# Performance work log

Hardware: AMD Instinct MI355X
Metric: run time of the kernel (lower is better)

The kernel has to match this reference:

```python
import jax, jax.numpy as jnp
import numpy as np

B, L, C, N = 64, 512, 1, 128  # batch, max seq len, num_conjugates, num_tags


def setup_inputs() -> dict:
    key = jax.random.key(0)
    k1, k2, k3, k4, k5 = jax.random.split(key, 5)
    emissions = jax.random.normal(k1, (B, L, C, N), dtype=jnp.float32)
    transitions = jax.random.normal(k2, (C, N, N), dtype=jnp.float32) * 0.01
    start_transitions = jax.random.normal(k3, (C, N), dtype=jnp.float32) * 0.01
    end_transitions = jax.random.normal(k4, (C, N), dtype=jnp.float32) * 0.01
    lengths = jax.random.randint(k5, (B,), 1, L + 1)  # valid lengths in [1, L]
    return {
        "emissions": emissions,
        "transitions": transitions,
        "start_transitions": start_transitions,
        "end_transitions": end_transitions,
        "lengths": lengths,
    }


def reference(emissions, transitions, start_transitions, end_transitions, lengths):
    # CRF log-partition (forward algorithm in the log semiring).
    # emissions: [B, L, C, N]; transitions: [C, N, N]; start/end: [C, N]; lengths: [B]
    b, l, c, n = emissions.shape
    # alpha_0 = start + emission at t=0  -> [B, C, N]
    alpha0 = start_transitions[None, :, :] + emissions[:, 0]

    e_rest = jnp.moveaxis(emissions[:, 1:], 1, 0)  # [L-1, B, C, N]
    t_idx = jnp.arange(1, l)

    def step(alpha, inp):
        e_t, t = inp
        # log-semiring mat-vec: logsumexp over previous tag axis
        scores = alpha[..., :, None] + transitions[None] + e_t[..., None, :]  # [B,C,N,N]
        new_alpha = jax.nn.logsumexp(scores, axis=2)  # [B, C, N]
        active = (t < lengths)[:, None, None]  # ragged mask: freeze finished sequences
        return jnp.where(active, new_alpha, alpha), None

    alpha, _ = jax.lax.scan(step, alpha0, (e_rest, t_idx))
    # terminate with end transitions -> log partition per (batch, conjugate)
    return jax.nn.logsumexp(alpha + end_transitions[None, :, :], axis=-1)  # [B, C]
```

## Files before the change

kernel.cpp:

```cpp
#include <hip/hip_runtime.h>


#define LOG2E 1.4426950408889634f
#define LN2   0.6931471805599453f

#define LDS_BARRIER() asm volatile("s_waitcnt lgkmcnt(0)\n\ts_barrier" ::: "memory")

typedef float    f2 __attribute__((ext_vector_type(2)));
typedef _Float16 h2 __attribute__((ext_vector_type(2)));

#define PKRTZ(a, b) __builtin_bit_cast(h2, __builtin_amdgcn_cvt_pkrtz((a), (b)))

template <int CTRL>
__device__ __forceinline__ float dpp_f(float x) {
    return __int_as_float(
        __builtin_amdgcn_mov_dpp(__float_as_int(x), CTRL, 0xF, 0xF, false));
}

__global__ __launch_bounds__(256)
__attribute__((amdgpu_waves_per_eu(1, 1)))
void crf_halves(
    const float* __restrict__ emissions,
    const float* __restrict__ transitions,
    const float* __restrict__ start_t,
    const float* __restrict__ end_t,
    const int*   __restrict__ lengths,
    float* __restrict__ wsV,
    int*   __restrict__ wsO)
{
    constexpr int N = 128;
    constexpr int L = 512;
    const int  bid = blockIdx.x;
    const bool isf = bid < 64;
    const int  b   = isf ? bid : bid - 64;
    const int  tid = threadIdx.x;
    const int  g   = tid >> 2;
    const int  k   = tid & 3;

    __shared__ alignas(16) float pbuf[2][80];

    h2 EA_0,  EA_1,  EA_2,  EA_3,  EA_4,  EA_5,  EA_6,  EA_7;
    h2 EA_8,  EA_9,  EA_10, EA_11, EA_12, EA_13, EA_14, EA_15;
    h2 EB_0,  EB_1,  EB_2,  EB_3,  EB_4,  EB_5,  EB_6,  EB_7;
    h2 EB_8,  EB_9,  EB_10, EB_11, EB_12, EB_13, EB_14, EB_15;
    if (isf) {
        const float* tb = transitions + (size_t)(32 * k) * N + 2 * g;
#define INIT_F(m)                                                              \
        {                                                                      \
            f2 r0 = *reinterpret_cast<const f2*>(tb + (size_t)(2 * (m)) * N);  \
            f2 r1 = *reinterpret_cast<const f2*>(tb + (size_t)(2 * (m) + 1) * N); \
            EA_##m = PKRTZ(__builtin_amdgcn_exp2f(r0.x * LOG2E),               \
                           __builtin_amdgcn_exp2f(r1.x * LOG2E));              \
            EB_##m = PKRTZ(__builtin_amdgcn_exp2f(r0.y * LOG2E),               \
                           __builtin_amdgcn_exp2f(r1.y * LOG2E));              \
        }
        INIT_F(0)  INIT_F(1)  INIT_F(2)  INIT_F(3)
        INIT_F(4)  INIT_F(5)  INIT_F(6)  INIT_F(7)
        INIT_F(8)  INIT_F(9)  INIT_F(10) INIT_F(11)
        INIT_F(12) INIT_F(13) INIT_F(14) INIT_F(15)
#undef INIT_F
    } else {
        const float* ra_ = transitions + (size_t)(2 * g) * N + 32 * k;
        const float* rb_ = transitions + (size_t)(2 * g + 1) * N + 32 * k;
#define INIT_B(m)                                                              \
        {                                                                      \
            f2 r0 = *reinterpret_cast<const f2*>(ra_ + 2 * (m));               \
            f2 r1 = *reinterpret_cast<const f2*>(rb_ + 2 * (m));               \
            EA_##m = PKRTZ(__builtin_amdgcn_exp2f(r0.x * LOG2E),               \
                           __builtin_amdgcn_exp2f(r0.y * LOG2E));              \
            EB_##m = PKRTZ(__builtin_amdgcn_exp2f(r1.x * LOG2E),               \
                           __builtin_amdgcn_exp2f(r1.y * LOG2E));              \
        }
        INIT_B(0)  INIT_B(1)  INIT_B(2)  INIT_B(3)
        INIT_B(4)  INIT_B(5)  INIT_B(6)  INIT_B(7)
        INIT_B(8)  INIT_B(9)  INIT_B(10) INIT_B(11)
        INIT_B(12) INIT_B(13) INIT_B(14) INIT_B(15)
#undef INIT_B
    }

    const int len = lengths[b];
    const int m   = (len - 1) >> 1;
    const float* eb = emissions + (size_t)b * L * N;

    int n_steps, e0, dstep; bool zfinal;
    if (isf) {
        n_steps = m; e0 = 1; dstep = 1; zfinal = false;
    } else {
        int total = len - 1 - m;
        n_steps = total > 0 ? total - 1 : 0;
        e0 = len - 2; if (e0 < 0) e0 = 0;
        dstep = -1;
        zfinal = total > 0;
    }

    int o = 0, cur = 0;
    float qA, qB;
    {
        const float* base = isf ? start_t : end_t;
        f2 bt = *reinterpret_cast<const f2*>(base + 2 * g);
        f2 ev;
        if (isf)         ev = *reinterpret_cast<const f2*>(eb + 2 * g);
        else if (zfinal) ev = *reinterpret_cast<const f2*>(eb + (size_t)(len - 1) * N + 2 * g);
        else           { ev.x = 0.f; ev.y = 0.f; }
        qA = __builtin_amdgcn_exp2f((bt.x + ev.x) * LOG2E);
        qB = __builtin_amdgcn_exp2f((bt.y + ev.y) * LOG2E);
        if (k == 0)
            pbuf[0][(g >> 4) * 20 + (g & 15)] =
                __builtin_bit_cast(float, PKRTZ(qA, qB));
    }
    LDS_BARRIER();

    auto eidx = [&](int n) {
        int nn = (n < n_steps) ? n : (n_steps - 1);
        if (nn < 0) nn = 0;
        return e0 + dstep * nn;
    };
    auto ldE = [&](int tt) {
        return *reinterpret_cast<const f2*>(eb + (size_t)tt * N + 2 * g);
    };

    auto STEP = [&](f2 ecur) {
        float q0w = pbuf[cur][0];
        const float4* pv = reinterpret_cast<const float4*>(&pbuf[cur][k * 20]);
        float4 Q0 = pv[0], Q1 = pv[1], Q2 = pv[2], Q3 = pv[3];

        unsigned u0 = __float_as_uint(q0w);
        int eS = (int)((u0 >> 10) & 0x1Fu) - 15;
        o += eS;
        float feS = (float)eS;
        float esA = __builtin_amdgcn_exp2f(ecur.x * LOG2E - feS);
        float esB = __builtin_amdgcn_exp2f(ecur.y * LOG2E - feS);

        float aA0 = 0.f, aA1 = 0.f, aB0 = 0.f, aB1 = 0.f;
#define D0(m_, Qc)                                                             \
        {                                                                      \
            h2 pm = __builtin_bit_cast(h2, Qc);                                \
            aA0 = __builtin_amdgcn_fdot2(pm, EA_##m_, aA0, false);             \
            aB0 = __builtin_amdgcn_fdot2(pm, EB_##m_, aB0, false);             \
        }
#define D1(m_, Qc)                                                             \
        {                                                                      \
            h2 pm = __builtin_bit_cast(h2, Qc);                                \
            aA1 = __builtin_amdgcn_fdot2(pm, EA_##m_, aA1, false);             \
            aB1 = __builtin_amdgcn_fdot2(pm, EB_##m_, aB1, false);             \
        }
        D0(0,  Q0.x) D1(1,  Q0.y) D0(2,  Q0.z) D1(3,  Q0.w)
        D0(4,  Q1.x) D1(5,  Q1.y) D0(6,  Q1.z) D1(7,  Q1.w)
        D0(8,  Q2.x) D1(9,  Q2.y) D0(10, Q2.z) D1(11, Q2.w)
        D0(12, Q3.x) D1(13, Q3.y) D0(14, Q3.z) D1(15, Q3.w)
#undef D0
#undef D1
        float dA = aA0 + aA1;
        float dB = aB0 + aB1;

        dA += dpp_f<0xB1>(dA); dB += dpp_f<0xB1>(dB);
        dA += dpp_f<0x4E>(dA); dB += dpp_f<0x4E>(dB);

        qA = esA * dA;
        qB = esB * dB;
        cur ^= 1;
        if (k == 0)
            pbuf[cur][(g >> 4) * 20 + (g & 15)] =
                __builtin_bit_cast(float, PKRTZ(qA, qB));
        LDS_BARRIER();
    };

    f2 ra = ldE(eidx(0));
    f2 rb = ldE(eidx(1));
    f2 rc = ldE(eidx(2));
    f2 rd = ldE(eidx(3));

    int n = 0;
    while (n < n_steps) {
        STEP(ra); ra = ldE(eidx(n + 4)); ++n; if (n >= n_steps) break;
        STEP(rb); rb = ldE(eidx(n + 4)); ++n; if (n >= n_steps) break;
        STEP(rc); rc = ldE(eidx(n + 4)); ++n; if (n >= n_steps) break;
        STEP(rd); rd = ldE(eidx(n + 4)); ++n;
    }
    if (zfinal) {
        f2 z; z.x = 0.f; z.y = 0.f;
        STEP(z);
    }

    float* wv = wsV + (size_t)((isf ? 0 : 64) + b) * 128;
    if (k == 0) {
        f2 q; q.x = qA; q.y = qB;
        *reinterpret_cast<f2*>(wv + 2 * g) = q;
    }
    if (tid == 0) wsO[(isf ? 0 : 64) + b] = o;
}

__global__ __launch_bounds__(64)
void crf_combine(const float* __restrict__ wsV, const int* __restrict__ wsO,
                 const int* __restrict__ lengths, float* __restrict__ out)
{
    const int b = blockIdx.x;
    const int g = threadIdx.x;
    f2 a = *reinterpret_cast<const f2*>(wsV + (size_t)b * 128 + 2 * g);
    f2 x = *reinterpret_cast<const f2*>(wsV + (size_t)(64 + b) * 128 + 2 * g);
    float v = a.x * x.x + a.y * x.y;
    #pragma unroll
    for (int s = 1; s < 64; s <<= 1) v += __shfl_xor(v, s);
    if (g == 0)
        out[b] = LN2 * ((float)(wsO[b] + wsO[64 + b]) +
                        __builtin_amdgcn_logf(v));
}

extern "C" void kernel_launch(void* const* d_in, const int* in_sizes, int n_in,
                              void* d_out, int out_size, void* d_ws, size_t ws_size,
                              hipStream_t stream) {
    const float* emissions   = (const float*)d_in[0];
    const float* transitions = (const float*)d_in[1];
    const float* start_t     = (const float*)d_in[2];
    const float* end_t       = (const float*)d_in[3];
    const int*   lengths     = (const int*)d_in[4];
    float* out = (float*)d_out;

    float* wsV = (float*)d_ws;
    int*   wsO = (int*)((char*)d_ws + 2 * 64 * 128 * sizeof(float));

    crf_halves<<<dim3(128), dim3(256), 0, stream>>>(
        emissions, transitions, start_t, end_t, lengths, wsV, wsO);
    crf_combine<<<dim3(64), dim3(64), 0, stream>>>(wsV, wsO, lengths, out);
}
```

Measured before the change: 131.5 us.

## Run each CRF half-chain in a single wavefront without block barriers

Each block shrinks from 256 threads to a single 64-lane wavefront. Every lane now holds all 64 fp16 transition pairs for its two tags and performs the full 128-term dot product itself, which replaces the DPP cross-lane reduction and the s_barrier with a plain LDS waitcnt, since a single wave needs no block barrier. The aim is to shorten the serial per-step latency chain. In exchange each lane does 4x more fdot2 work and reads all 64 packed alphas from LDS every step. The 128 transition registers per lane also raise register pressure and the risk of spilling.

```diff
diff --git a/kernel.cpp b/kernel.cpp
--- a/kernel.cpp
+++ b/kernel.cpp
@@ -4,20 +4,15 @@
 #define LOG2E 1.4426950408889634f
 #define LN2   0.6931471805599453f
 
-#define LDS_BARRIER() asm volatile("s_waitcnt lgkmcnt(0)\n\ts_barrier" ::: "memory")
+#define LGKM0() asm volatile("s_waitcnt lgkmcnt(0)" ::: "memory")
 
 typedef float    f2 __attribute__((ext_vector_type(2)));
+typedef float    f4 __attribute__((ext_vector_type(4)));
 typedef _Float16 h2 __attribute__((ext_vector_type(2)));
 
 #define PKRTZ(a, b) __builtin_bit_cast(h2, __builtin_amdgcn_cvt_pkrtz((a), (b)))
 
-template <int CTRL>
-__device__ __forceinline__ float dpp_f(float x) {
-    return __int_as_float(
-        __builtin_amdgcn_mov_dpp(__float_as_int(x), CTRL, 0xF, 0xF, false));
-}
-
-__global__ __launch_bounds__(256)
+__global__ __launch_bounds__(64)
 __attribute__((amdgpu_waves_per_eu(1, 1)))
 void crf_halves(
     const float* __restrict__ emissions,
@@ -33,49 +28,34 @@
     const int  bid = blockIdx.x;
     const bool isf = bid < 64;
     const int  b   = isf ? bid : bid - 64;
-    const int  tid = threadIdx.x;
-    const int  g   = tid >> 2;
-    const int  k   = tid & 3;
+    const int  p   = threadIdx.x;
 
-    __shared__ alignas(16) float pbuf[2][80];
+    __shared__ alignas(16) float pbuf[2][64];
 
-    h2 EA_0,  EA_1,  EA_2,  EA_3,  EA_4,  EA_5,  EA_6,  EA_7;
-    h2 EA_8,  EA_9,  EA_10, EA_11, EA_12, EA_13, EA_14, EA_15;
-    h2 EB_0,  EB_1,  EB_2,  EB_3,  EB_4,  EB_5,  EB_6,  EB_7;
-    h2 EB_8,  EB_9,  EB_10, EB_11, EB_12, EB_13, EB_14, EB_15;
+    h2 EA[64], EB[64];
     if (isf) {
-        const float* tb = transitions + (size_t)(32 * k) * N + 2 * g;
-#define INIT_F(m)                                                              \
-        {                                                                      \
-            f2 r0 = *reinterpret_cast<const f2*>(tb + (size_t)(2 * (m)) * N);  \
-            f2 r1 = *reinterpret_cast<const f2*>(tb + (size_t)(2 * (m) + 1) * N); \
-            EA_##m = PKRTZ(__builtin_amdgcn_exp2f(r0.x * LOG2E),               \
-                           __builtin_amdgcn_exp2f(r1.x * LOG2E));              \
-            EB_##m = PKRTZ(__builtin_amdgcn_exp2f(r0.y * LOG2E),               \
-                           __builtin_amdgcn_exp2f(r1.y * LOG2E));              \
+        const float* tb = transitions + 2 * p;
+        #pragma unroll
+        for (int m = 0; m < 64; ++m) {
+            f2 r0 = *reinterpret_cast<const f2*>(tb + (size_t)(2 * m) * N);
+            f2 r1 = *reinterpret_cast<const f2*>(tb + (size_t)(2 * m + 1) * N);
+            EA[m] = PKRTZ(__builtin_amdgcn_exp2f(r0.x * LOG2E),
+                          __builtin_amdgcn_exp2f(r1.x * LOG2E));
+            EB[m] = PKRTZ(__builtin_amdgcn_exp2f(r0.y * LOG2E),
+                          __builtin_amdgcn_exp2f(r1.y * LOG2E));
         }
-        INIT_F(0)  INIT_F(1)  INIT_F(2)  INIT_F(3)
-        INIT_F(4)  INIT_F(5)  INIT_F(6)  INIT_F(7)
-        INIT_F(8)  INIT_F(9)  INIT_F(10) INIT_F(11)
-        INIT_F(12) INIT_F(13) INIT_F(14) INIT_F(15)
-#undef INIT_F
     } else {
-        const float* ra_ = transitions + (size_t)(2 * g) * N + 32 * k;
-        const float* rb_ = transitions + (size_t)(2 * g + 1) * N + 32 * k;
-#define INIT_B(m)                                                              \
-        {                                                                      \
-            f2 r0 = *reinterpret_cast<const f2*>(ra_ + 2 * (m));               \
-            f2 r1 = *reinterpret_cast<const f2*>(rb_ + 2 * (m));               \
-            EA_##m = PKRTZ(__builtin_amdgcn_exp2f(r0.x * LOG2E),               \
-                           __builtin_amdgcn_exp2f(r0.y * LOG2E));              \
-            EB_##m = PKRTZ(__builtin_amdgcn_exp2f(r1.x * LOG2E),               \
-                           __builtin_amdgcn_exp2f(r1.y * LOG2E));              \
+        const float* ra_ = transitions + (size_t)(2 * p) * N;
+        const float* rb_ = ra_ + N;
+        #pragma unroll
+        for (int m = 0; m < 64; ++m) {
+            f2 r0 = *reinterpret_cast<const f2*>(ra_ + 2 * m);
+            f2 r1 = *reinterpret_cast<const f2*>(rb_ + 2 * m);
+            EA[m] = PKRTZ(__builtin_amdgcn_exp2f(r0.x * LOG2E),
+                          __builtin_amdgcn_exp2f(r0.y * LOG2E));
+            EB[m] = PKRTZ(__builtin_amdgcn_exp2f(r1.x * LOG2E),
+                          __builtin_amdgcn_exp2f(r1.y * LOG2E));
         }
-        INIT_B(0)  INIT_B(1)  INIT_B(2)  INIT_B(3)
-        INIT_B(4)  INIT_B(5)  INIT_B(6)  INIT_B(7)
-        INIT_B(8)  INIT_B(9)  INIT_B(10) INIT_B(11)
-        INIT_B(12) INIT_B(13) INIT_B(14) INIT_B(15)
-#undef INIT_B
     }
 
     const int len = lengths[b];
@@ -97,18 +77,16 @@
     float qA, qB;
     {
         const float* base = isf ? start_t : end_t;
-        f2 bt = *reinterpret_cast<const f2*>(base + 2 * g);
+        f2 bt = *reinterpret_cast<const f2*>(base + 2 * p);
         f2 ev;
-        if (isf)         ev = *reinterpret_cast<const f2*>(eb + 2 * g);
-        else if (zfinal) ev = *reinterpret_cast<const f2*>(eb + (size_t)(len - 1) * N + 2 * g);
+        if (isf)         ev = *reinterpret_cast<const f2*>(eb + 2 * p);
+        else if (zfinal) ev = *reinterpret_cast<const f2*>(eb + (size_t)(len - 1) * N + 2 * p);
         else           { ev.x = 0.f; ev.y = 0.f; }
         qA = __builtin_amdgcn_exp2f((bt.x + ev.x) * LOG2E);
         qB = __builtin_amdgcn_exp2f((bt.y + ev.y) * LOG2E);
-        if (k == 0)
-            pbuf[0][(g >> 4) * 20 + (g & 15)] =
-                __builtin_bit_cast(float, PKRTZ(qA, qB));
+        pbuf[0][p] = __builtin_bit_cast(float, PKRTZ(qA, qB));
     }
-    LDS_BARRIER();
+    LGKM0();
 
     auto eidx = [&](int n) {
         int nn = (n < n_steps) ? n : (n_steps - 1);
@@ -116,53 +94,38 @@
         return e0 + dstep * nn;
     };
     auto ldE = [&](int tt) {
-        return *reinterpret_cast<const f2*>(eb + (size_t)tt * N + 2 * g);
+        return *reinterpret_cast<const f2*>(eb + (size_t)tt * N + 2 * p);
     };
 
     auto STEP = [&](f2 ecur) {
-        float q0w = pbuf[cur][0];
-        const float4* pv = reinterpret_cast<const float4*>(&pbuf[cur][k * 20]);
-        float4 Q0 = pv[0], Q1 = pv[1], Q2 = pv[2], Q3 = pv[3];
+        const f4* pv = reinterpret_cast<const f4*>(&pbuf[cur][0]);
+        f4 P[16];
+        #pragma unroll
+        for (int r = 0; r < 16; ++r) P[r] = pv[r];
 
-        unsigned u0 = __float_as_uint(q0w);
+        unsigned u0 = __float_as_uint(P[0][0]);
         int eS = (int)((u0 >> 10) & 0x1Fu) - 15;
         o += eS;
         float feS = (float)eS;
         float esA = __builtin_amdgcn_exp2f(ecur.x * LOG2E - feS);
         float esB = __builtin_amdgcn_exp2f(ecur.y * LOG2E - feS);
 
-        float aA0 = 0.f, aA1 = 0.f, aB0 = 0.f, aB1 = 0.f;
-#define D0(m_, Qc)                                                             \
-        {                                                                      \
-            h2 pm = __builtin_bit_cast(h2, Qc);                                \
-            aA0 = __builtin_amdgcn_fdot2(pm, EA_##m_, aA0, false);             \
-            aB0 = __builtin_amdgcn_fdot2(pm, EB_##m_, aB0, false);             \
+        float aA[4] = {0.f, 0.f, 0.f, 0.f};
+        float aB[4] = {0.f, 0.f, 0.f, 0.f};
+        #pragma unroll
+        for (int mm = 0; mm < 64; ++mm) {
+            h2 pm = __builtin_bit_cast(h2, P[mm >> 2][mm & 3]);
+            aA[mm & 3] = __builtin_amdgcn_fdot2(pm, EA[mm], aA[mm & 3], false);
+            aB[mm & 3] = __builtin_amdgcn_fdot2(pm, EB[mm], aB[mm & 3], false);
         }
-#define D1(m_, Qc)                                                             \
-        {                                                                      \
-            h2 pm = __builtin_bit_cast(h2, Qc);                                \
-            aA1 = __builtin_amdgcn_fdot2(pm, EA_##m_, aA1, false);             \
-            aB1 = __builtin_amdgcn_fdot2(pm, EB_##m_, aB1, false);             \
-        }
-        D0(0,  Q0.x) D1(1,  Q0.y) D0(2,  Q0.z) D1(3,  Q0.w)
-        D0(4,  Q1.x) D1(5,  Q1.y) D0(6,  Q1.z) D1(7,  Q1.w)
-        D0(8,  Q2.x) D1(9,  Q2.y) D0(10, Q2.z) D1(11, Q2.w)
-        D0(12, Q3.x) D1(13, Q3.y) D0(14, Q3.z) D1(15, Q3.w)
-#undef D0
-#undef D1
-        float dA = aA0 + aA1;
-        float dB = aB0 + aB1;
-
-        dA += dpp_f<0xB1>(dA); dB += dpp_f<0xB1>(dB);
-        dA += dpp_f<0x4E>(dA); dB += dpp_f<0x4E>(dB);
+        float dA = (aA[0] + aA[1]) + (aA[2] + aA[3]);
+        float dB = (aB[0] + aB[1]) + (aB[2] + aB[3]);
 
         qA = esA * dA;
         qB = esB * dB;
         cur ^= 1;
-        if (k == 0)
-            pbuf[cur][(g >> 4) * 20 + (g & 15)] =
-                __builtin_bit_cast(float, PKRTZ(qA, qB));
-        LDS_BARRIER();
+        pbuf[cur][p] = __builtin_bit_cast(float, PKRTZ(qA, qB));
+        LGKM0();
     };
 
     f2 ra = ldE(eidx(0));
@@ -183,11 +146,9 @@
     }
 
     float* wv = wsV + (size_t)((isf ? 0 : 64) + b) * 128;
-    if (k == 0) {
-        f2 q; q.x = qA; q.y = qB;
-        *reinterpret_cast<f2*>(wv + 2 * g) = q;
-    }
-    if (tid == 0) wsO[(isf ? 0 : 64) + b] = o;
+    f2 q; q.x = qA; q.y = qB;
+    *reinterpret_cast<f2*>(wv + 2 * p) = q;
+    if (p == 0) wsO[(isf ? 0 : 64) + b] = o;
 }
 
 __global__ __launch_bounds__(64)
@@ -219,7 +180,7 @@
     float* wsV = (float*)d_ws;
     int*   wsO = (int*)((char*)d_ws + 2 * 64 * 128 * sizeof(float));
 
-    crf_halves<<<dim3(128), dim3(256), 0, stream>>>(
+    crf_halves<<<dim3(128), dim3(64), 0, stream>>>(
         emissions, transitions, start_t, end_t, lengths, wsV, wsO);
     crf_combine<<<dim3(64), dim3(64), 0, stream>>>(wsV, wsO, lengths, out);
 }
```

New measurement: 228.3 us. 73.6% more time.

## Interleave two batch sequences per block to hide per-step barrier latency

Applied to the files above, without the earlier changes.

Each block now advances two independent batch sequences (b and b+32) in lockstep. They share one LDS barrier per step and their dot-product chains are interleaved, so the latency-bound recurrence gets twice the independent work between barriers. The grid drops from 128 to 64 blocks. The loop now runs to the longer of the two sequences, so the shorter one idles under per-round guards, and the extra live registers add pressure.

```diff
diff --git a/kernel.cpp b/kernel.cpp
--- a/kernel.cpp
+++ b/kernel.cpp
@@ -31,13 +31,16 @@
     constexpr int N = 128;
     constexpr int L = 512;
     const int  bid = blockIdx.x;
-    const bool isf = bid < 64;
-    const int  b   = isf ? bid : bid - 64;
+    const bool isf = bid < 32;
+    const int  s   = isf ? bid : bid - 32;
+    const int  b1  = s;
+    const int  b2  = s + 32;
     const int  tid = threadIdx.x;
     const int  g   = tid >> 2;
     const int  k   = tid & 3;
 
-    __shared__ alignas(16) float pbuf[2][80];
+    __shared__ alignas(16) float pb1[2][80];
+    __shared__ alignas(16) float pb2[2][80];
 
     h2 EA_0,  EA_1,  EA_2,  EA_3,  EA_4,  EA_5,  EA_6,  EA_7;
     h2 EA_8,  EA_9,  EA_10, EA_11, EA_12, EA_13, EA_14, EA_15;
@@ -78,116 +81,163 @@
 #undef INIT_B
     }
 
-    const int len = lengths[b];
-    const int m   = (len - 1) >> 1;
-    const float* eb = emissions + (size_t)b * L * N;
-
-    int n_steps, e0, dstep; bool zfinal;
+    const int len1 = lengths[b1];
+    const int len2 = lengths[b2];
+    const int m1   = (len1 - 1) >> 1;
+    const int m2   = (len2 - 1) >> 1;
+    const float* eb1 = emissions + (size_t)b1 * L * N;
+    const float* eb2 = emissions + (size_t)b2 * L * N;
+
+    int ns1, e01, total1, ns2, e02, total2, dstep;
     if (isf) {
-        n_steps = m; e0 = 1; dstep = 1; zfinal = false;
+        dstep = 1;
+        ns1 = m1; e01 = 1; total1 = m1;
+        ns2 = m2; e02 = 1; total2 = m2;
     } else {
-        int total = len - 1 - m;
-        n_steps = total > 0 ? total - 1 : 0;
-        e0 = len - 2; if (e0 < 0) e0 = 0;
         dstep = -1;
-        zfinal = total > 0;
-    }
-
-    int o = 0, cur = 0;
-    float qA, qB;
+        int tt1 = len1 - 1 - m1;
+        ns1 = tt1 > 0 ? tt1 - 1 : 0; e01 = len1 - 2 < 0 ? 0 : len1 - 2; total1 = tt1;
+        int tt2 = len2 - 1 - m2;
+        ns2 = tt2 > 0 ? tt2 - 1 : 0; e02 = len2 - 2 < 0 ? 0 : len2 - 2; total2 = tt2;
+    }
+
+    int o1 = 0, o2 = 0, cur = 0;
+    float qA1, qB1, qA2, qB2;
     {
         const float* base = isf ? start_t : end_t;
         f2 bt = *reinterpret_cast<const f2*>(base + 2 * g);
-        f2 ev;
-        if (isf)         ev = *reinterpret_cast<const f2*>(eb + 2 * g);
-        else if (zfinal) ev = *reinterpret_cast<const f2*>(eb + (size_t)(len - 1) * N + 2 * g);
-        else           { ev.x = 0.f; ev.y = 0.f; }
-        qA = __builtin_amdgcn_exp2f((bt.x + ev.x) * LOG2E);
-        qB = __builtin_amdgcn_exp2f((bt.y + ev.y) * LOG2E);
-        if (k == 0)
-            pbuf[0][(g >> 4) * 20 + (g & 15)] =
-                __builtin_bit_cast(float, PKRTZ(qA, qB));
+        f2 ev1, ev2;
+        if (isf) {
+            ev1 = *reinterpret_cast<const f2*>(eb1 + 2 * g);
+            ev2 = *reinterpret_cast<const f2*>(eb2 + 2 * g);
+        } else {
+            if (len1 > 1) ev1 = *reinterpret_cast<const f2*>(eb1 + (size_t)(len1 - 1) * N + 2 * g);
+            else        { ev1.x = 0.f; ev1.y = 0.f; }
+            if (len2 > 1) ev2 = *reinterpret_cast<const f2*>(eb2 + (size_t)(len2 - 1) * N + 2 * g);
+            else        { ev2.x = 0.f; ev2.y = 0.f; }
+        }
+        qA1 = __builtin_amdgcn_exp2f((bt.x + ev1.x) * LOG2E);
+        qB1 = __builtin_amdgcn_exp2f((bt.y + ev1.y) * LOG2E);
+        qA2 = __builtin_amdgcn_exp2f((bt.x + ev2.x) * LOG2E);
+        qB2 = __builtin_amdgcn_exp2f((bt.y + ev2.y) * LOG2E);
+        if (k == 0) {
+            pb1[0][(g >> 4) * 20 + (g & 15)] = __builtin_bit_cast(float, PKRTZ(qA1, qB1));
+            pb2[0][(g >> 4) * 20 + (g & 15)] = __builtin_bit_cast(float, PKRTZ(qA2, qB2));
+        }
     }
     LDS_BARRIER();
 
-    auto eidx = [&](int n) {
-        int nn = (n < n_steps) ? n : (n_steps - 1);
+    auto ei1 = [&](int n) {
+        int nn = (n < ns1) ? n : (ns1 - 1);
         if (nn < 0) nn = 0;
-        return e0 + dstep * nn;
-    };
-    auto ldE = [&](int tt) {
-        return *reinterpret_cast<const f2*>(eb + (size_t)tt * N + 2 * g);
-    };
-
-    auto STEP = [&](f2 ecur) {
-        float q0w = pbuf[cur][0];
-        const float4* pv = reinterpret_cast<const float4*>(&pbuf[cur][k * 20]);
-        float4 Q0 = pv[0], Q1 = pv[1], Q2 = pv[2], Q3 = pv[3];
-
-        unsigned u0 = __float_as_uint(q0w);
-        int eS = (int)((u0 >> 10) & 0x1Fu) - 15;
-        o += eS;
-        float feS = (float)eS;
-        float esA = __builtin_amdgcn_exp2f(ecur.x * LOG2E - feS);
-        float esB = __builtin_amdgcn_exp2f(ecur.y * LOG2E - feS);
-
+        return e01 + dstep * nn;
+    };
+    auto ei2 = [&](int n) {
+        int nn = (n < ns2) ? n : (ns2 - 1);
+        if (nn < 0) nn = 0;
+        return e02 + dstep * nn;
+    };
+    auto ldE1 = [&](int tt) {
+        return *reinterpret_cast<const f2*>(eb1 + (size_t)tt * N + 2 * g);
+    };
+    auto ldE2 = [&](int tt) {
+        return *reinterpret_cast<const f2*>(eb2 + (size_t)tt * N + 2 * g);
+    };
+
+    auto DOT = [&](const float4& Qa, const float4& Qb, const float4& Qc,
+                   const float4& Qd, float& dA, float& dB) {
         float aA0 = 0.f, aA1 = 0.f, aB0 = 0.f, aB1 = 0.f;
-#define D0(m_, Qc)                                                             \
-        {                                                                      \
-            h2 pm = __builtin_bit_cast(h2, Qc);                                \
+#define D0(m_, Qc_)                                                            \
+        {                                                                      \
+            h2 pm = __builtin_bit_cast(h2, Qc_);                               \
             aA0 = __builtin_amdgcn_fdot2(pm, EA_##m_, aA0, false);             \
             aB0 = __builtin_amdgcn_fdot2(pm, EB_##m_, aB0, false);             \
         }
-#define D1(m_, Qc)                                                             \
-        {                                                                      \
-            h2 pm = __builtin_bit_cast(h2, Qc);                                \
+#define D1(m_, Qc_)                                                            \
+        {                                                                      \
+            h2 pm = __builtin_bit_cast(h2, Qc_);                               \
             aA1 = __builtin_amdgcn_fdot2(pm, EA_##m_, aA1, false);             \
             aB1 = __builtin_amdgcn_fdot2(pm, EB_##m_, aB1, false);             \
         }
-        D0(0,  Q0.x) D1(1,  Q0.y) D0(2,  Q0.z) D1(3,  Q0.w)
-        D0(4,  Q1.x) D1(5,  Q1.y) D0(6,  Q1.z) D1(7,  Q1.w)
-        D0(8,  Q2.x) D1(9,  Q2.y) D0(10, Q2.z) D1(11, Q2.w)
-        D0(12, Q3.x) D1(13, Q3.y) D0(14, Q3.z) D1(15, Q3.w)
+        D0(0,  Qa.x) D1(1,  Qa.y) D0(2,  Qa.z) D1(3,  Qa.w)
+        D0(4,  Qb.x) D1(5,  Qb.y) D0(6,  Qb.z) D1(7,  Qb.w)
+        D0(8,  Qc.x) D1(9,  Qc.y) D0(10, Qc.z) D1(11, Qc.w)
+        D0(12, Qd.x) D1(13, Qd.y) D0(14, Qd.z) D1(15, Qd.w)
 #undef D0
 #undef D1
-        float dA = aA0 + aA1;
-        float dB = aB0 + aB1;
-
-        dA += dpp_f<0xB1>(dA); dB += dpp_f<0xB1>(dB);
-        dA += dpp_f<0x4E>(dA); dB += dpp_f<0x4E>(dB);
-
-        qA = esA * dA;
-        qB = esB * dB;
+        float dA_ = aA0 + aA1;
+        float dB_ = aB0 + aB1;
+        dA_ += dpp_f<0xB1>(dA_); dB_ += dpp_f<0xB1>(dB_);
+        dA_ += dpp_f<0x4E>(dA_); dB_ += dpp_f<0x4E>(dB_);
+        dA = dA_; dB = dB_;
+    };
+
+    auto ROUND = [&](f2 e1, f2 e2, int r) {
+        float q0w1 = pb1[cur][0];
+        const float4* pv1 = reinterpret_cast<const float4*>(&pb1[cur][k * 20]);
+        float4 Qa1 = pv1[0], Qb1 = pv1[1], Qc1 = pv1[2], Qd1 = pv1[3];
+        float q0w2 = pb2[cur][0];
+        const float4* pv2 = reinterpret_cast<const float4*>(&pb2[cur][k * 20]);
+        float4 Qa2 = pv2[0], Qb2 = pv2[1], Qc2 = pv2[2], Qd2 = pv2[3];
+
+        float dA1, dB1, dA2, dB2;
+        DOT(Qa1, Qb1, Qc1, Qd1, dA1, dB1);
+        DOT(Qa2, Qb2, Qc2, Qd2, dA2, dB2);
+
+        if (r < total1) {
+            unsigned u0 = __float_as_uint(q0w1);
+            int eS = (int)((u0 >> 10) & 0x1Fu) - 15;
+            o1 += eS;
+            float feS = (float)eS;
+            f2 ec = e1;
+            if (r >= ns1) { ec.x = 0.f; ec.y = 0.f; }
+            qA1 = __builtin_amdgcn_exp2f(ec.x * LOG2E - feS) * dA1;
+            qB1 = __builtin_amdgcn_exp2f(ec.y * LOG2E - feS) * dB1;
+        }
+        if (r < total2) {
+            unsigned u0 = __float_as_uint(q0w2);
+            int eS = (int)((u0 >> 10) & 0x1Fu) - 15;
+            o2 += eS;
+            float feS = (float)eS;
+            f2 ec = e2;
+            if (r >= ns2) { ec.x = 0.f; ec.y = 0.f; }
+            qA2 = __builtin_amdgcn_exp2f(ec.x * LOG2E - feS) * dA2;
+            qB2 = __builtin_amdgcn_exp2f(ec.y * LOG2E - feS) * dB2;
+        }
         cur ^= 1;
-        if (k == 0)
-            pbuf[cur][(g >> 4) * 20 + (g & 15)] =
-                __builtin_bit_cast(float, PKRTZ(qA, qB));
+        if (k == 0) {
+            pb1[cur][(g >> 4) * 20 + (g & 15)] = __builtin_bit_cast(float, PKRTZ(qA1, qB1));
+            pb2[cur][(g >> 4) * 20 + (g & 15)] = __builtin_bit_cast(float, PKRTZ(qA2, qB2));
+        }
         LDS_BARRIER();
     };
 
-    f2 ra = ldE(eidx(0));
-    f2 rb = ldE(eidx(1));
-    f2 rc = ldE(eidx(2));
-    f2 rd = ldE(eidx(3));
-
-    int n = 0;
-    while (n < n_steps) {
-        STEP(ra); ra = ldE(eidx(n + 4)); ++n; if (n >= n_steps) break;
-        STEP(rb); rb = ldE(eidx(n + 4)); ++n; if (n >= n_steps) break;
-        STEP(rc); rc = ldE(eidx(n + 4)); ++n; if (n >= n_steps) break;
-        STEP(rd); rd = ldE(eidx(n + 4)); ++n;
-    }
-    if (zfinal) {
-        f2 z; z.x = 0.f; z.y = 0.f;
-        STEP(z);
-    }
-
-    float* wv = wsV + (size_t)((isf ? 0 : 64) + b) * 128;
-    if (k == 0) {
-        f2 q; q.x = qA; q.y = qB;
-        *reinterpret_cast<f2*>(wv + 2 * g) = q;
-    }
-    if (tid == 0) wsO[(isf ? 0 : 64) + b] = o;
+    f2 ra1 = ldE1(ei1(0)), rb1 = ldE1(ei1(1)), rc1 = ldE1(ei1(2)), rd1 = ldE1(ei1(3));
+    f2 ra2 = ldE2(ei2(0)), rb2 = ldE2(ei2(1)), rc2 = ldE2(ei2(2)), rd2 = ldE2(ei2(3));
+
+    const int R = total1 > total2 ? total1 : total2;
+    int r = 0;
+    while (r < R) {
+        ROUND(ra1, ra2, r); ra1 = ldE1(ei1(r + 4)); ra2 = ldE2(ei2(r + 4)); ++r; if (r >= R) break;
+        ROUND(rb1, rb2, r); rb1 = ldE1(ei1(r + 4)); rb2 = ldE2(ei2(r + 4)); ++r; if (r >= R) break;
+        ROUND(rc1, rc2, r); rc1 = ldE1(ei1(r + 4)); rc2 = ldE2(ei2(r + 4)); ++r; if (r >= R) break;
+        ROUND(rd1, rd2, r); rd1 = ldE1(ei1(r + 4)); rd2 = ldE2(ei2(r + 4)); ++r;
+    }
+
+    {
+        float* wv1 = wsV + (size_t)((isf ? 0 : 64) + b1) * 128;
+        float* wv2 = wsV + (size_t)((isf ? 0 : 64) + b2) * 128;
+        if (k == 0) {
+            f2 q1; q1.x = qA1; q1.y = qB1;
+            f2 q2; q2.x = qA2; q2.y = qB2;
+            *reinterpret_cast<f2*>(wv1 + 2 * g) = q1;
+            *reinterpret_cast<f2*>(wv2 + 2 * g) = q2;
+        }
+        if (tid == 0) {
+            wsO[(isf ? 0 : 64) + b1] = o1;
+            wsO[(isf ? 0 : 64) + b2] = o2;
+        }
+    }
 }
 
 __global__ __launch_bounds__(64)
@@ -219,7 +269,7 @@
     float* wsV = (float*)d_ws;
     int*   wsO = (int*)((char*)d_ws + 2 * 64 * 128 * sizeof(float));
 
-    crf_halves<<<dim3(128), dim3(256), 0, stream>>>(
+    crf_halves<<<dim3(64), dim3(256), 0, stream>>>(
         emissions, transitions, start_t, end_t, lengths, wsV, wsO);
     crf_combine<<<dim3(64), dim3(64), 0, stream>>>(wsV, wsO, lengths, out);
 }
```

After: 184.1 us. 40.1% more time.

## Remap CRF step so each wave owns a k-slice and reduces partials via LDS

Applied to the files above, without the earlier changes.

Work is remapped so each of the four waves owns a 32-row slice of the previous-tag axis and each lane owns two output tags. The previous alpha vector is gathered with ds_bpermute from the lane's own packed fp16 value instead of being broadcast through LDS. Cross-wave partial sums are then combined through one LDS write, a barrier and vector reads, replacing the DPP quad reduction. The goal is to shorten the per-step serial critical path (LDS store, barrier, LDS load), at the cost of 16 bpermutes per step and a larger LDS reduction buffer.

```diff
diff --git a/kernel.cpp b/kernel.cpp
--- a/kernel.cpp
+++ b/kernel.cpp
@@ -7,15 +7,10 @@
 #define LDS_BARRIER() asm volatile("s_waitcnt lgkmcnt(0)\n\ts_barrier" ::: "memory")
 
 typedef float    f2 __attribute__((ext_vector_type(2)));
+typedef float    f4 __attribute__((ext_vector_type(4)));
 typedef _Float16 h2 __attribute__((ext_vector_type(2)));
 
 #define PKRTZ(a, b) __builtin_bit_cast(h2, __builtin_amdgcn_cvt_pkrtz((a), (b)))
-
-template <int CTRL>
-__device__ __forceinline__ float dpp_f(float x) {
-    return __int_as_float(
-        __builtin_amdgcn_mov_dpp(__float_as_int(x), CTRL, 0xF, 0xF, false));
-}
 
 __global__ __launch_bounds__(256)
 __attribute__((amdgpu_waves_per_eu(1, 1)))
@@ -34,24 +29,24 @@
     const bool isf = bid < 64;
     const int  b   = isf ? bid : bid - 64;
     const int  tid = threadIdx.x;
-    const int  g   = tid >> 2;
-    const int  k   = tid & 3;
-
-    __shared__ alignas(16) float pbuf[2][80];
+    const int  w   = tid >> 6;
+    const int  l   = tid & 63;
+
+    __shared__ alignas(16) float P_red[2][64][8];
 
     h2 EA_0,  EA_1,  EA_2,  EA_3,  EA_4,  EA_5,  EA_6,  EA_7;
     h2 EA_8,  EA_9,  EA_10, EA_11, EA_12, EA_13, EA_14, EA_15;
     h2 EB_0,  EB_1,  EB_2,  EB_3,  EB_4,  EB_5,  EB_6,  EB_7;
     h2 EB_8,  EB_9,  EB_10, EB_11, EB_12, EB_13, EB_14, EB_15;
     if (isf) {
-        const float* tb = transitions + (size_t)(32 * k) * N + 2 * g;
-#define INIT_F(m)                                                              \
+        const float* tb = transitions + (size_t)(32 * w) * N + 2 * l;
+#define INIT_F(j)                                                              \
         {                                                                      \
-            f2 r0 = *reinterpret_cast<const f2*>(tb + (size_t)(2 * (m)) * N);  \
-            f2 r1 = *reinterpret_cast<const f2*>(tb + (size_t)(2 * (m) + 1) * N); \
-            EA_##m = PKRTZ(__builtin_amdgcn_exp2f(r0.x * LOG2E),               \
+            f2 r0 = *reinterpret_cast<const f2*>(tb + (size_t)(2 * (j)) * N);  \
+            f2 r1 = *reinterpret_cast<const f2*>(tb + (size_t)(2 * (j) + 1) * N); \
+            EA_##j = PKRTZ(__builtin_amdgcn_exp2f(r0.x * LOG2E),               \
                            __builtin_amdgcn_exp2f(r1.x * LOG2E));              \
-            EB_##m = PKRTZ(__builtin_amdgcn_exp2f(r0.y * LOG2E),               \
+            EB_##j = PKRTZ(__builtin_amdgcn_exp2f(r0.y * LOG2E),               \
                            __builtin_amdgcn_exp2f(r1.y * LOG2E));              \
         }
         INIT_F(0)  INIT_F(1)  INIT_F(2)  INIT_F(3)
@@ -60,15 +55,15 @@
         INIT_F(12) INIT_F(13) INIT_F(14) INIT_F(15)
 #undef INIT_F
     } else {
-        const float* ra_ = transitions + (size_t)(2 * g) * N + 32 * k;
-        const float* rb_ = transitions + (size_t)(2 * g + 1) * N + 32 * k;
-#define INIT_B(m)                                                              \
+        const float* ra_ = transitions + (size_t)(2 * l) * N + 32 * w;
+        const float* rb_ = transitions + (size_t)(2 * l + 1) * N + 32 * w;
+#define INIT_B(j)                                                              \
         {                                                                      \
-            f2 r0 = *reinterpret_cast<const f2*>(ra_ + 2 * (m));               \
-            f2 r1 = *reinterpret_cast<const f2*>(rb_ + 2 * (m));               \
-            EA_##m = PKRTZ(__builtin_amdgcn_exp2f(r0.x * LOG2E),               \
+            f2 r0 = *reinterpret_cast<const f2*>(ra_ + 2 * (j));               \
+            f2 r1 = *reinterpret_cast<const f2*>(rb_ + 2 * (j));               \
+            EA_##j = PKRTZ(__builtin_amdgcn_exp2f(r0.x * LOG2E),               \
                            __builtin_amdgcn_exp2f(r0.y * LOG2E));              \
-            EB_##m = PKRTZ(__builtin_amdgcn_exp2f(r1.x * LOG2E),               \
+            EB_##j = PKRTZ(__builtin_amdgcn_exp2f(r1.x * LOG2E),               \
                            __builtin_amdgcn_exp2f(r1.y * LOG2E));              \
         }
         INIT_B(0)  INIT_B(1)  INIT_B(2)  INIT_B(3)
@@ -95,20 +90,19 @@
 
     int o = 0, cur = 0;
     float qA, qB;
+    int qpk, sq0;
     {
         const float* base = isf ? start_t : end_t;
-        f2 bt = *reinterpret_cast<const f2*>(base + 2 * g);
+        f2 bt = *reinterpret_cast<const f2*>(base + 2 * l);
         f2 ev;
-        if (isf)         ev = *reinterpret_cast<const f2*>(eb + 2 * g);
-        else if (zfinal) ev = *reinterpret_cast<const f2*>(eb + (size_t)(len - 1) * N + 2 * g);
+        if (isf)         ev = *reinterpret_cast<const f2*>(eb + 2 * l);
+        else if (zfinal) ev = *reinterpret_cast<const f2*>(eb + (size_t)(len - 1) * N + 2 * l);
         else           { ev.x = 0.f; ev.y = 0.f; }
         qA = __builtin_amdgcn_exp2f((bt.x + ev.x) * LOG2E);
         qB = __builtin_amdgcn_exp2f((bt.y + ev.y) * LOG2E);
-        if (k == 0)
-            pbuf[0][(g >> 4) * 20 + (g & 15)] =
-                __builtin_bit_cast(float, PKRTZ(qA, qB));
-    }
-    LDS_BARRIER();
+        qpk = __builtin_bit_cast(int, PKRTZ(qA, qB));
+        sq0 = __builtin_amdgcn_readfirstlane(qpk);
+    }
 
     auto eidx = [&](int n) {
         int nn = (n < n_steps) ? n : (n_steps - 1);
@@ -116,53 +110,62 @@
         return e0 + dstep * nn;
     };
     auto ldE = [&](int tt) {
-        return *reinterpret_cast<const f2*>(eb + (size_t)tt * N + 2 * g);
+        return *reinterpret_cast<const f2*>(eb + (size_t)tt * N + 2 * l);
     };
 
     auto STEP = [&](f2 ecur) {
-        float q0w = pbuf[cur][0];
-        const float4* pv = reinterpret_cast<const float4*>(&pbuf[cur][k * 20]);
-        float4 Q0 = pv[0], Q1 = pv[1], Q2 = pv[2], Q3 = pv[3];
-
-        unsigned u0 = __float_as_uint(q0w);
-        int eS = (int)((u0 >> 10) & 0x1Fu) - 15;
+        int P0  = __builtin_amdgcn_ds_bpermute((16 * w + 0)  * 4, qpk);
+        int P1  = __builtin_amdgcn_ds_bpermute((16 * w + 1)  * 4, qpk);
+        int P2  = __builtin_amdgcn_ds_bpermute((16 * w + 2)  * 4, qpk);
+        int P3  = __builtin_amdgcn_ds_bpermute((16 * w + 3)  * 4, qpk);
+        int P4  = __builtin_amdgcn_ds_bpermute((16 * w + 4)  * 4, qpk);
+        int P5  = __builtin_amdgcn_ds_bpermute((16 * w + 5)  * 4, qpk);
+        int P6  = __builtin_amdgcn_ds_bpermute((16 * w + 6)  * 4, qpk);
+        int P7  = __builtin_amdgcn_ds_bpermute((16 * w + 7)  * 4, qpk);
+        int P8  = __builtin_amdgcn_ds_bpermute((16 * w + 8)  * 4, qpk);
+        int P9  = __builtin_amdgcn_ds_bpermute((16 * w + 9)  * 4, qpk);
+        int P10 = __builtin_amdgcn_ds_bpermute((16 * w + 10) * 4, qpk);
+        int P11 = __builtin_amdgcn_ds_bpermute((16 * w + 11) * 4, qpk);
+        int P12 = __builtin_amdgcn_ds_bpermute((16 * w + 12) * 4, qpk);
+        int P13 = __builtin_amdgcn_ds_bpermute((16 * w + 13) * 4, qpk);
+        int P14 = __builtin_amdgcn_ds_bpermute((16 * w + 14) * 4, qpk);
+        int P15 = __builtin_amdgcn_ds_bpermute((16 * w + 15) * 4, qpk);
+
+        int eS = ((sq0 >> 10) & 31) - 15;
         o += eS;
         float feS = (float)eS;
         float esA = __builtin_amdgcn_exp2f(ecur.x * LOG2E - feS);
         float esB = __builtin_amdgcn_exp2f(ecur.y * LOG2E - feS);
 
         float aA0 = 0.f, aA1 = 0.f, aB0 = 0.f, aB1 = 0.f;
-#define D0(m_, Qc)                                                             \
+#define DJ(j0, j1, Pa, Pb)                                                     \
         {                                                                      \
-            h2 pm = __builtin_bit_cast(h2, Qc);                                \
-            aA0 = __builtin_amdgcn_fdot2(pm, EA_##m_, aA0, false);             \
-            aB0 = __builtin_amdgcn_fdot2(pm, EB_##m_, aB0, false);             \
+            h2 pa = __builtin_bit_cast(h2, Pa);                                \
+            h2 pb = __builtin_bit_cast(h2, Pb);                                \
+            aA0 = __builtin_amdgcn_fdot2(pa, EA_##j0, aA0, false);             \
+            aB0 = __builtin_amdgcn_fdot2(pa, EB_##j0, aB0, false);             \
+            aA1 = __builtin_amdgcn_fdot2(pb, EA_##j1, aA1, false);             \
+            aB1 = __builtin_amdgcn_fdot2(pb, EB_##j1, aB1, false);             \
         }
-#define D1(m_, Qc)                                                             \
-        {                                                                      \
-            h2 pm = __builtin_bit_cast(h2, Qc);                                \
-            aA1 = __builtin_amdgcn_fdot2(pm, EA_##m_, aA1, false);             \
-            aB1 = __builtin_amdgcn_fdot2(pm, EB_##m_, aB1, false);             \
-        }
-        D0(0,  Q0.x) D1(1,  Q0.y) D0(2,  Q0.z) D1(3,  Q0.w)
-        D0(4,  Q1.x) D1(5,  Q1.y) D0(6,  Q1.z) D1(7,  Q1.w)
-        D0(8,  Q2.x) D1(9,  Q2.y) D0(10, Q2.z) D1(11, Q2.w)
-        D0(12, Q3.x) D1(13, Q3.y) D0(14, Q3.z) D1(15, Q3.w)
-#undef D0
-#undef D1
-        float dA = aA0 + aA1;
-        float dB = aB0 + aB1;
-
-        dA += dpp_f<0xB1>(dA); dB += dpp_f<0xB1>(dB);
-        dA += dpp_f<0x4E>(dA); dB += dpp_f<0x4E>(dB);
+        DJ(0,  1,  P0,  P1)  DJ(2,  3,  P2,  P3)
+        DJ(4,  5,  P4,  P5)  DJ(6,  7,  P6,  P7)
+        DJ(8,  9,  P8,  P9)  DJ(10, 11, P10, P11)
+        DJ(12, 13, P12, P13) DJ(14, 15, P14, P15)
+#undef DJ
+
+        f2 part; part.x = aA0 + aA1; part.y = aB0 + aB1;
+        cur ^= 1;
+        *reinterpret_cast<f2*>(&P_red[cur][l][2 * w]) = part;
+        LDS_BARRIER();
+        f4 r01 = *reinterpret_cast<const f4*>(&P_red[cur][l][0]);
+        f4 r23 = *reinterpret_cast<const f4*>(&P_red[cur][l][4]);
+        float dA = (r01.x + r01.z) + (r23.x + r23.z);
+        float dB = (r01.y + r01.w) + (r23.y + r23.w);
 
         qA = esA * dA;
         qB = esB * dB;
-        cur ^= 1;
-        if (k == 0)
-            pbuf[cur][(g >> 4) * 20 + (g & 15)] =
-                __builtin_bit_cast(float, PKRTZ(qA, qB));
-        LDS_BARRIER();
+        qpk = __builtin_bit_cast(int, PKRTZ(qA, qB));
+        sq0 = __builtin_amdgcn_readfirstlane(qpk);
     };
 
     f2 ra = ldE(eidx(0));
@@ -182,10 +185,10 @@
         STEP(z);
     }
 
-    float* wv = wsV + (size_t)((isf ? 0 : 64) + b) * 128;
-    if (k == 0) {
+    if (w == 0) {
+        float* wv = wsV + (size_t)((isf ? 0 : 64) + b) * 128;
         f2 q; q.x = qA; q.y = qB;
-        *reinterpret_cast<f2*>(wv + 2 * g) = q;
+        *reinterpret_cast<f2*>(wv + 2 * l) = q;
     }
     if (tid == 0) wsO[(isf ? 0 : 64) + b] = o;
 }
```

Measured after the change: 167.8 us. +27.6%, slower.
